# Kernel optimization log

Measured on AMD Instinct MI355X. Metric: run time of the kernel, lower is better.

Reference implementation:

```python
import jax, jax.numpy as jnp
import numpy as np

WS = 7           # window size (module init window_size=(7,7))
HEADS = 8
LN_EPS = 1e-5


def _relative_position_index(ws: int) -> np.ndarray:
    # Exactly mirrors the torch buffer construction in __init__.
    ch = np.arange(ws)
    coords = np.stack(np.meshgrid(ch, ch, indexing='ij'))          # [2, ws, ws]
    cf = coords.reshape(2, -1)                                     # [2, ws*ws]
    rel = cf[:, :, None] - cf[:, None, :]                          # [2, N, N]
    rel = rel.transpose(1, 2, 0).copy()                            # [N, N, 2]
    rel[:, :, 0] += ws - 1
    rel[:, :, 1] += ws - 1
    rel[:, :, 0] *= 2 * ws - 1
    return rel.sum(-1)                                             # [N, N] in [0, 169)


def setup_inputs() -> dict:
    key = jax.random.key(0)
    ks = jax.random.split(key, 5)
    B, H, W, C = 4, 224, 224, 256
    return {
        'x': jax.random.normal(ks[0], (B, H, W, C), jnp.float32),
        'w_qkv': jax.random.normal(ks[1], (C, 3 * C), jnp.float32) * 0.02,
        'b_qkv': jnp.zeros((3 * C,), jnp.float32),
        'bias_table': jax.random.normal(ks[2], ((2 * WS - 1) ** 2, HEADS), jnp.float32) * 0.02,
        'w_out': jax.random.normal(ks[3], (C, C), jnp.float32) * 0.02,
        'b_out': jnp.zeros((C,), jnp.float32),
        'ln_gamma': jnp.ones((C,), jnp.float32),
        'ln_beta': jnp.zeros((C,), jnp.float32),
    }


def reference(x, w_qkv, b_qkv, bias_table, w_out, b_out, ln_gamma, ln_beta):
    B, H, W, C = x.shape
    hd = C // HEADS
    scale = (HEADS // 2) ** -0.5          # faithful: head_dim = heads // 2 in source
    N = WS * WS

    # window partition: (B,H,W,C) -> (nW, WS*WS, C)
    xw = x.reshape(B, H // WS, WS, W // WS, WS, C)
    xw = xw.transpose(0, 1, 3, 2, 4, 5).reshape(-1, N, C)
    nW = xw.shape[0]

    # fused QKV projection
    qkv = xw @ w_qkv + b_qkv                                        # [nW, N, 3C]
    qkv = qkv.reshape(nW, N, 3, HEADS, hd).transpose(2, 0, 3, 1, 4)  # [3, nW, h, N, hd]
    q, k, v = qkv[0], qkv[1], qkv[2]

    # relative position bias gather: [N, N, heads] -> [heads, N, N]
    rel_idx = _relative_position_index(WS)                          # numpy constant
    bias = bias_table[rel_idx.reshape(-1)].reshape(N, N, HEADS).transpose(2, 0, 1)

    attn = jnp.einsum('whqd,whkd->whqk', q, k) * scale + bias[None]  # [nW, h, N, N]
    attn = jax.nn.softmax(attn, axis=-1)

    out = jnp.einsum('whqk,whkd->whqd', attn, v)                    # [nW, h, N, hd]
    out = out.transpose(0, 2, 1, 3).reshape(nW, N, C)
    out = out @ w_out + b_out

    # residual + layernorm (temporal_tokens + cur_tokens -> LayerNorm)
    y = out + xw
    mean = y.mean(-1, keepdims=True)
    var = ((y - mean) ** 2).mean(-1, keepdims=True)
    y = (y - mean) * jax.lax.rsqrt(var + LN_EPS) * ln_gamma + ln_beta
    return y.reshape(-1, C)                                          # [nW*N, C] tokens
```

## Files before the change

kernel.cpp:

```cpp
#include <hip/hip_runtime.h>
#include <hip/hip_bf16.h>

#define BATCH 4
#define IMG 224
#define CDIM 256
#define WS 7
#define NWIN 4096
#define NTOK 49
#define TTOK 200704
#define HEADS 8
#define HD 32
#define SCALE 0.5f
#define LN_EPS 1e-5f

typedef __attribute__((ext_vector_type(8))) short short8v;
typedef __attribute__((ext_vector_type(4))) float f32x4;
typedef unsigned short u16;

__device__ __forceinline__ u16 f2bf(float f) {
  __hip_bfloat16 h = __float2bfloat16(f);
  return *reinterpret_cast<u16*>(&h);
}

__device__ __forceinline__ void gld_lds16(const void* g, void* l) {
  __builtin_amdgcn_global_load_lds(
      (const __attribute__((address_space(1))) unsigned int*)g,
      (__attribute__((address_space(3))) unsigned int*)l, 16, 0, 0);
}

__global__ __launch_bounds__(256) void pack_x(const float* __restrict__ x,
                                              u16* __restrict__ xb) {
  const int NCH = TTOK * 32;
  for (int id = blockIdx.x * 256 + threadIdx.x; id < NCH; id += 2048 * 256) {
    int t = id >> 5;
    int cc = (id & 31) << 3;
    int wq = t / 49, n = t - wq * 49;
    int b = wq >> 10, rem = wq & 1023;
    int gh = (rem >> 5) * 7 + n / 7;
    int gw = (rem & 31) * 7 + n % 7;
    const float* src = x + (((size_t)b * IMG + gh) * IMG + gw) * CDIM + cc;
    float4 f0 = *(const float4*)src;
    float4 f1 = *(const float4*)(src + 4);
    union { u16 us[8]; uint4 v; } pk;
    pk.us[0] = f2bf(f0.x); pk.us[1] = f2bf(f0.y);
    pk.us[2] = f2bf(f0.z); pk.us[3] = f2bf(f0.w);
    pk.us[4] = f2bf(f1.x); pk.us[5] = f2bf(f1.y);
    pk.us[6] = f2bf(f1.z); pk.us[7] = f2bf(f1.w);
    *(uint4*)(xb + (size_t)id * 8) = pk.v;
  }
}

__global__ __launch_bounds__(256) void pack_w(const float* __restrict__ wqkv,
                                              const float* __restrict__ wout,
                                              u16* __restrict__ wqkvT,
                                              u16* __restrict__ woutT) {
  int id = blockIdx.x * 256 + threadIdx.x;
  if (id < 196608) {
    int nn = id >> 8, k = id & 255;
    wqkvT[id] = f2bf(wqkv[(size_t)k * 768 + nn]);
  } else {
    int id2 = id - 196608;
    int nn = id2 >> 8, k = id2 & 255;
    woutT[id2] = f2bf(wout[(size_t)k * 256 + nn]);
  }
}

__global__ __launch_bounds__(256) void qkv_gemm(const u16* __restrict__ xb,
                                                const u16* __restrict__ wqkvT,
                                                const float* __restrict__ bqkv,
                                                u16* __restrict__ qkvb) {
  __shared__ __align__(16) short As[2][4096];
  __shared__ __align__(16) short Bs[2][4096];

  int tid = threadIdx.x;
  int lane = tid & 63, wid = tid >> 6;
  int wm = wid >> 1, wn = wid & 1;
  int hb = blockIdx.x;
  int bid = (hb & 7) * 1176 + (hb >> 3);
  int mt = bid / 6, nt = bid % 6;
  int m0 = mt * 128, n0 = nt * 128;

  f32x4 zero = {0.f, 0.f, 0.f, 0.f};
  f32x4 acc[4][4];
#pragma unroll
  for (int m = 0; m < 4; ++m)
#pragma unroll
    for (int n = 0; n < 4; ++n) acc[m][n] = zero;

#define STAGE_K1(buf, k0)                                                \
  {                                                                      \
    _Pragma("unroll") for (int i = 0; i < 2; ++i) {                      \
      int c = i * 256 + tid;                                             \
      int l6 = c & 63;                                                   \
      int rr = ((c >> 6) << 4) + (l6 & 15);                              \
      int kk = (k0) + ((l6 >> 4) << 3);                                  \
      gld_lds16(xb + (size_t)(m0 + rr) * 256 + kk, &As[buf][c * 8]);     \
      gld_lds16(wqkvT + (size_t)(n0 + rr) * 256 + kk, &Bs[buf][c * 8]);  \
    }                                                                    \
  }

  STAGE_K1(0, 0);
  __syncthreads();

  int buf = 0;
  for (int ks = 0; ks < 8; ++ks) {
    if (ks < 7) STAGE_K1(buf ^ 1, (ks + 1) * 32);
    short8v af[4], bfv[4];
#pragma unroll
    for (int m = 0; m < 4; ++m)
      af[m] = *(const short8v*)&As[buf][((wm * 4 + m) * 64 + lane) * 8];
#pragma unroll
    for (int n = 0; n < 4; ++n)
      bfv[n] = *(const short8v*)&Bs[buf][((wn * 4 + n) * 64 + lane) * 8];
#pragma unroll
    for (int m = 0; m < 4; ++m)
#pragma unroll
      for (int n = 0; n < 4; ++n)
        acc[m][n] = __builtin_amdgcn_mfma_f32_16x16x32_bf16(af[m], bfv[n],
                                                            acc[m][n], 0, 0, 0);
    __syncthreads();
    buf ^= 1;
  }

  int fr = lane & 15, fq = lane >> 4;
#pragma unroll
  for (int n = 0; n < 4; ++n) {
    int c = n0 + wn * 64 + n * 16 + fr;
    float bias = bqkv[c];
    u16* plane = qkvb + (size_t)((c >> 8) * 8 + ((c >> 5) & 7)) * TTOK * 32;
    int d = c & 31;
#pragma unroll
    for (int m = 0; m < 4; ++m) {
      int t0 = m0 + wm * 64 + m * 16 + fq * 4;
#pragma unroll
      for (int r = 0; r < 4; ++r)
        plane[(size_t)(t0 + r) * 32 + d] = f2bf(acc[m][n][r] + bias);
    }
  }
}

__global__ __launch_bounds__(256) void attn_kernel(
    const u16* __restrict__ qkvb, const float* __restrict__ bias_table,
    u16* __restrict__ attnb) {
  __shared__ u16 Pl[4][4096];
  __shared__ u16 Vl[4][32 * 72];
  __shared__ float bsh[4][169];

  int bid = blockIdx.x;
  int w = bid >> 1;
  int wid = threadIdx.x >> 6, lane = threadIdx.x & 63;
  int h = ((bid & 1) << 2) | wid;
  int cl = lane & 15, cg = lane >> 4;

  for (int i = lane; i < 169; i += 64)
    bsh[wid][i] = bias_table[i * HEADS + h];

  const size_t wbase = (size_t)w * 49 * 32;
  const u16* qp = qkvb + (size_t)h * TTOK * 32 + wbase;
  const u16* kp = qkvb + (size_t)(8 + h) * TTOK * 32 + wbase;
  const u16* vp = qkvb + (size_t)(16 + h) * TTOK * 32 + wbase;

  short8v qf[4], kf[4];
#pragma unroll
  for (int mt = 0; mt < 4; ++mt) {
    int off = (mt * 16 + cl) * 32 + cg * 8;
    qf[mt] = *(const short8v*)(qp + off);
    kf[mt] = *(const short8v*)(kp + off);
  }

  short8v vz = {0, 0, 0, 0, 0, 0, 0, 0};
#pragma unroll
  for (int pass = 0; pass < 4; ++pass) {
    int cidx = pass * 64 + lane;
    int t = cidx >> 2, dc = (cidx & 3) * 8;
    short8v vv = (t < 49) ? *(const short8v*)(vp + t * 32 + dc) : vz;
#pragma unroll
    for (int j = 0; j < 8; ++j) Vl[wid][(dc + j) * 72 + t] = vv[j];
  }

  f32x4 zero4 = {0.f, 0.f, 0.f, 0.f};
  f32x4 s[4][4];
#pragma unroll
  for (int mt = 0; mt < 4; ++mt)
#pragma unroll
    for (int nt = 0; nt < 4; ++nt)
      s[mt][nt] = __builtin_amdgcn_mfma_f32_16x16x32_bf16(qf[mt], kf[nt],
                                                          zero4, 0, 0, 0);

  int kr7[4], kc7[4];
#pragma unroll
  for (int nt = 0; nt < 4; ++nt) {
    int col = nt * 16 + cl;
    kr7[nt] = (col * 9363) >> 16;
    kc7[nt] = col - kr7[nt] * 7;
  }

  f32x4 rinv[4];
#pragma unroll
  for (int mt = 0; mt < 4; ++mt) {
#pragma unroll
    for (int r = 0; r < 4; ++r) {
      int row = mt * 16 + cg * 4 + r;
      int qr = (row * 9363) >> 16;
      int qc = row - qr * 7;
      float sv[4];
#pragma unroll
      for (int nt = 0; nt < 4; ++nt) {
        int col = nt * 16 + cl;
        if (col < 49) {
          int idx = (qr - kr7[nt] + 6) * 13 + (qc - kc7[nt] + 6);
          sv[nt] = s[mt][nt][r] * SCALE + bsh[wid][idx];
        } else {
          sv[nt] = -1e30f;
        }
      }
      float m = fmaxf(fmaxf(sv[0], sv[1]), fmaxf(sv[2], sv[3]));
#pragma unroll
      for (int msk = 1; msk < 16; msk <<= 1) m = fmaxf(m, __shfl_xor(m, msk));
      float sum = 0.f;
#pragma unroll
      for (int nt = 0; nt < 4; ++nt) {
        float p = __expf(sv[nt] - m);
        s[mt][nt][r] = p;
        sum += p;
      }
#pragma unroll
      for (int msk = 1; msk < 16; msk <<= 1) sum += __shfl_xor(sum, msk);
      rinv[mt][r] = 1.0f / sum;
    }
  }

#pragma unroll
  for (int mt = 0; mt < 4; ++mt)
#pragma unroll
    for (int r = 0; r < 4; ++r) {
      int row = mt * 16 + cg * 4 + r;
      int swz = (row & 7) << 3;
#pragma unroll
      for (int nt = 0; nt < 4; ++nt) {
        int col = nt * 16 + cl;
        Pl[wid][(row * 64 + col) ^ swz] = f2bf(s[mt][nt][r]);
      }
    }

  f32x4 o[4][2];
#pragma unroll
  for (int mt = 0; mt < 4; ++mt)
#pragma unroll
    for (int nt2 = 0; nt2 < 2; ++nt2) o[mt][nt2] = zero4;

#pragma unroll
  for (int kt = 0; kt < 2; ++kt) {
    short8v vfr[2];
#pragma unroll
    for (int nt2 = 0; nt2 < 2; ++nt2)
      vfr[nt2] = *(const short8v*)&Vl[wid][(nt2 * 16 + cl) * 72 + kt * 32 + cg * 8];
#pragma unroll
    for (int mt = 0; mt < 4; ++mt) {
      int row = mt * 16 + cl;
      short8v pa = *(const short8v*)
          &Pl[wid][(row * 64 + kt * 32 + cg * 8) ^ ((row & 7) << 3)];
#pragma unroll
      for (int nt2 = 0; nt2 < 2; ++nt2)
        o[mt][nt2] = __builtin_amdgcn_mfma_f32_16x16x32_bf16(pa, vfr[nt2],
                                                             o[mt][nt2], 0, 0, 0);
    }
  }

#pragma unroll
  for (int mt = 0; mt < 4; ++mt)
#pragma unroll
    for (int r = 0; r < 4; ++r) {
      int row = mt * 16 + cg * 4 + r;
      if (row < 49) {
        float ri = rinv[mt][r];
        size_t dst = (size_t)(w * 49 + row) * 256 + h * 32;
#pragma unroll
        for (int nt2 = 0; nt2 < 2; ++nt2)
          attnb[dst + nt2 * 16 + cl] = f2bf(o[mt][nt2][r] * ri);
      }
    }
}

__global__ __launch_bounds__(512) void out_ln_kernel(
    const u16* __restrict__ attnb, const u16* __restrict__ woutT,
    const float* __restrict__ bout, const float* __restrict__ x,
    const float* __restrict__ gamma, const float* __restrict__ beta,
    float* __restrict__ out) {
  __shared__ __align__(16) short As[2][4096];
  __shared__ __align__(16) short Bs[2][8192];
  __shared__ float ls1[128], ls2[128];
  __shared__ int rowoff_s[128];

  int tid = threadIdx.x;
  int lane = tid & 63, wid = tid >> 6;
  int wm = wid >> 2, wn = wid & 3;
  int m0 = blockIdx.x * 128;

  if (tid < 128) {
    ls1[tid] = 0.f;
    ls2[tid] = 0.f;
    int t = m0 + tid;
    int wq = t / 49, n = t - wq * 49;
    int b = wq >> 10, rem = wq & 1023;
    int gh = (rem >> 5) * 7 + n / 7;
    int gw = (rem & 31) * 7 + n % 7;
    rowoff_s[tid] = ((b * IMG + gh) * IMG + gw) * CDIM;
  }

  f32x4 zero = {0.f, 0.f, 0.f, 0.f};
  f32x4 acc[4][4];
#pragma unroll
  for (int m = 0; m < 4; ++m)
#pragma unroll
    for (int n = 0; n < 4; ++n) acc[m][n] = zero;

#define STAGE_K3(buf, k0)                                                 \
  {                                                                       \
    {                                                                     \
      int c = tid;                                                        \
      int l6 = c & 63;                                                    \
      int rr = ((c >> 6) << 4) + (l6 & 15);                               \
      int kk = (k0) + ((l6 >> 4) << 3);                                   \
      gld_lds16(attnb + (size_t)(m0 + rr) * 256 + kk, &As[buf][c * 8]);   \
    }                                                                     \
    _Pragma("unroll") for (int i = 0; i < 2; ++i) {                       \
      int c = i * 512 + tid;                                              \
      int l6 = c & 63;                                                    \
      int cc = ((c >> 6) << 4) + (l6 & 15);                               \
      int kk = (k0) + ((l6 >> 4) << 3);                                   \
      gld_lds16(woutT + (size_t)cc * 256 + kk, &Bs[buf][c * 8]);          \
    }                                                                     \
  }

  STAGE_K3(0, 0);
  __syncthreads();

  int buf = 0;
  for (int ks = 0; ks < 8; ++ks) {
    if (ks < 7) STAGE_K3(buf ^ 1, (ks + 1) * 32);
    short8v af[4], bfv[4];
#pragma unroll
    for (int m = 0; m < 4; ++m)
      af[m] = *(const short8v*)&As[buf][((wm * 4 + m) * 64 + lane) * 8];
#pragma unroll
    for (int n = 0; n < 4; ++n)
      bfv[n] = *(const short8v*)&Bs[buf][((wn * 4 + n) * 64 + lane) * 8];
#pragma unroll
    for (int m = 0; m < 4; ++m)
#pragma unroll
      for (int n = 0; n < 4; ++n)
        acc[m][n] = __builtin_amdgcn_mfma_f32_16x16x32_bf16(af[m], bfv[n],
                                                            acc[m][n], 0, 0, 0);
    __syncthreads();
    buf ^= 1;
  }

  int fr = lane & 15, fq = lane >> 4;
#pragma unroll
  for (int m = 0; m < 4; ++m) {
#pragma unroll
    for (int r = 0; r < 4; ++r) {
      int lrow = wm * 64 + m * 16 + fq * 4 + r;
      const float* xr = x + rowoff_s[lrow];
      float s1 = 0.f, s2 = 0.f;
#pragma unroll
      for (int n = 0; n < 4; ++n) {
        int c = wn * 64 + n * 16 + fr;
        float v = acc[m][n][r] + bout[c] + xr[c];
        acc[m][n][r] = v;
        s1 += v;
        s2 += v * v;
      }
#pragma unroll
      for (int off = 1; off < 16; off <<= 1) {
        s1 += __shfl_xor(s1, off);
        s2 += __shfl_xor(s2, off);
      }
      if (fr == 0) {
        atomicAdd(&ls1[lrow], s1);
        atomicAdd(&ls2[lrow], s2);
      }
    }
  }
  __syncthreads();

#pragma unroll
  for (int m = 0; m < 4; ++m) {
#pragma unroll
    for (int r = 0; r < 4; ++r) {
      int lrow = wm * 64 + m * 16 + fq * 4 + r;
      float mean = ls1[lrow] * (1.0f / 256.0f);
      float var = ls2[lrow] * (1.0f / 256.0f) - mean * mean;
      float rstd = rsqrtf(var + LN_EPS);
      size_t orow = (size_t)(m0 + lrow) * 256;
#pragma unroll
      for (int n = 0; n < 4; ++n) {
        int c = wn * 64 + n * 16 + fr;
        out[orow + c] = (acc[m][n][r] - mean) * rstd * gamma[c] + beta[c];
      }
    }
  }
}

extern "C" void kernel_launch(void* const* d_in, const int* in_sizes, int n_in,
                              void* d_out, int out_size, void* d_ws, size_t ws_size,
                              hipStream_t stream) {
  const float* x     = (const float*)d_in[0];
  const float* wqkv  = (const float*)d_in[1];
  const float* bqkv  = (const float*)d_in[2];
  const float* btab  = (const float*)d_in[3];
  const float* wout  = (const float*)d_in[4];
  const float* bout  = (const float*)d_in[5];
  const float* gamma = (const float*)d_in[6];
  const float* beta  = (const float*)d_in[7];
  float* out = (float*)d_out;

  u16* qkvb  = (u16*)d_ws;
  u16* xb    = qkvb + (size_t)24 * TTOK * 32;
  u16* attnb = xb;
  u16* wqkvT = xb + (size_t)TTOK * 256;
  u16* woutT = wqkvT + 196608;

  pack_x<<<2048, 256, 0, stream>>>(x, xb);
  pack_w<<<1024, 256, 0, stream>>>(wqkv, wout, wqkvT, woutT);
  qkv_gemm<<<(TTOK / 128) * 6, 256, 0, stream>>>(xb, wqkvT, bqkv, qkvb);
  attn_kernel<<<NWIN * 2, 256, 0, stream>>>(qkvb, btab, attnb);
  out_ln_kernel<<<TTOK / 128, 512, 0, stream>>>(attnb, woutT, bout, x, gamma,
                                                beta, out);
}
```

Before: 922.6 us.

## Store QKV row-major with packed vector stores and preload full K in LDS

The QKV GEMM now swaps operand roles so each lane holds four consecutive output columns, which allows packed 8-byte stores into a token-major [token,768] QKV buffer instead of scattered 2-byte stores into per-head planes. The attention kernel is updated to read Q/K/V with a 768-element row stride. The GEMM also loads the whole K=256 extent into 128KB of LDS up front and drops the double-buffered pipeline and per-step barriers. This costs occupancy and removes load/compute overlap, and the attention loads become strided across rows.

Result: slower. 978.6 us (+6.1%).

```diff
diff --git a/kernel.cpp b/kernel.cpp
--- a/kernel.cpp
+++ b/kernel.cpp
@@ -69,72 +69,70 @@
                                                 const u16* __restrict__ wqkvT,
                                                 const float* __restrict__ bqkv,
                                                 u16* __restrict__ qkvb) {
-  __shared__ __align__(16) short As[2][4096];
-  __shared__ __align__(16) short Bs[2][4096];
+  __shared__ __align__(16) short As[32768];
+  __shared__ __align__(16) short Bs[32768];
 
   int tid = threadIdx.x;
   int lane = tid & 63, wid = tid >> 6;
-  int wm = wid >> 1, wn = wid & 1;
+  int wn = wid >> 1, wt = wid & 1;
   int hb = blockIdx.x;
   int bid = (hb & 7) * 1176 + (hb >> 3);
   int mt = bid / 6, nt = bid % 6;
   int m0 = mt * 128, n0 = nt * 128;
 
+#pragma unroll
+  for (int ks = 0; ks < 8; ++ks) {
+#pragma unroll
+    for (int i = 0; i < 2; ++i) {
+      int c = i * 256 + tid;
+      int l6 = c & 63;
+      int rr = ((c >> 6) << 4) + (l6 & 15);
+      int kk = ks * 32 + ((l6 >> 4) << 3);
+      gld_lds16(wqkvT + (size_t)(n0 + rr) * 256 + kk, &As[ks * 4096 + c * 8]);
+      gld_lds16(xb + (size_t)(m0 + rr) * 256 + kk, &Bs[ks * 4096 + c * 8]);
+    }
+  }
+
   f32x4 zero = {0.f, 0.f, 0.f, 0.f};
   f32x4 acc[4][4];
 #pragma unroll
-  for (int m = 0; m < 4; ++m)
-#pragma unroll
-    for (int n = 0; n < 4; ++n) acc[m][n] = zero;
-
-#define STAGE_K1(buf, k0)                                                \
-  {                                                                      \
-    _Pragma("unroll") for (int i = 0; i < 2; ++i) {                      \
-      int c = i * 256 + tid;                                             \
-      int l6 = c & 63;                                                   \
-      int rr = ((c >> 6) << 4) + (l6 & 15);                              \
-      int kk = (k0) + ((l6 >> 4) << 3);                                  \
-      gld_lds16(xb + (size_t)(m0 + rr) * 256 + kk, &As[buf][c * 8]);     \
-      gld_lds16(wqkvT + (size_t)(n0 + rr) * 256 + kk, &Bs[buf][c * 8]);  \
-    }                                                                    \
-  }
-
-  STAGE_K1(0, 0);
+  for (int n = 0; n < 4; ++n)
+#pragma unroll
+    for (int t = 0; t < 4; ++t) acc[n][t] = zero;
+
   __syncthreads();
 
-  int buf = 0;
+#pragma unroll
   for (int ks = 0; ks < 8; ++ks) {
-    if (ks < 7) STAGE_K1(buf ^ 1, (ks + 1) * 32);
     short8v af[4], bfv[4];
 #pragma unroll
-    for (int m = 0; m < 4; ++m)
-      af[m] = *(const short8v*)&As[buf][((wm * 4 + m) * 64 + lane) * 8];
-#pragma unroll
     for (int n = 0; n < 4; ++n)
-      bfv[n] = *(const short8v*)&Bs[buf][((wn * 4 + n) * 64 + lane) * 8];
-#pragma unroll
-    for (int m = 0; m < 4; ++m)
-#pragma unroll
-      for (int n = 0; n < 4; ++n)
-        acc[m][n] = __builtin_amdgcn_mfma_f32_16x16x32_bf16(af[m], bfv[n],
-                                                            acc[m][n], 0, 0, 0);
-    __syncthreads();
-    buf ^= 1;
-  }
-
-  int fr = lane & 15, fq = lane >> 4;
+      af[n] = *(const short8v*)&As[ks * 4096 + ((wn * 4 + n) * 64 + lane) * 8];
+#pragma unroll
+    for (int t = 0; t < 4; ++t)
+      bfv[t] = *(const short8v*)&Bs[ks * 4096 + ((wt * 4 + t) * 64 + lane) * 8];
+#pragma unroll
+    for (int n = 0; n < 4; ++n)
+#pragma unroll
+      for (int t = 0; t < 4; ++t)
+        acc[n][t] = __builtin_amdgcn_mfma_f32_16x16x32_bf16(af[n], bfv[t],
+                                                            acc[n][t], 0, 0, 0);
+  }
+
+  int cl = lane & 15, fq = lane >> 4;
 #pragma unroll
   for (int n = 0; n < 4; ++n) {
-    int c = n0 + wn * 64 + n * 16 + fr;
-    float bias = bqkv[c];
-    u16* plane = qkvb + (size_t)((c >> 8) * 8 + ((c >> 5) & 7)) * TTOK * 32;
-    int d = c & 31;
-#pragma unroll
-    for (int m = 0; m < 4; ++m) {
-      int t0 = m0 + wm * 64 + m * 16 + fq * 4;
-#pragma unroll
-      for (int r = 0; r < 4; ++r)
-        plane[(size_t)(t0 + r) * 32 + d] = f2bf(acc[m][n][r] + bias);
+    int nb = n0 + wn * 64 + n * 16 + fq * 4;
+    float4 bq = *(const float4*)(bqkv + nb);
+#pragma unroll
+    for (int t = 0; t < 4; ++t) {
+      int tr = m0 + wt * 64 + t * 16 + cl;
+      union { u16 us[4]; uint2 v; } pk;
+      pk.us[0] = f2bf(acc[n][t][0] + bq.x);
+      pk.us[1] = f2bf(acc[n][t][1] + bq.y);
+      pk.us[2] = f2bf(acc[n][t][2] + bq.z);
+      pk.us[3] = f2bf(acc[n][t][3] + bq.w);
+      *(uint2*)(qkvb + (size_t)tr * 768 + nb) = pk.v;
     }
   }
 }
@@ -155,15 +153,15 @@
   for (int i = lane; i < 169; i += 64)
     bsh[wid][i] = bias_table[i * HEADS + h];
 
-  const size_t wbase = (size_t)w * 49 * 32;
-  const u16* qp = qkvb + (size_t)h * TTOK * 32 + wbase;
-  const u16* kp = qkvb + (size_t)(8 + h) * TTOK * 32 + wbase;
-  const u16* vp = qkvb + (size_t)(16 + h) * TTOK * 32 + wbase;
+  const u16* rowb = qkvb + (size_t)w * 49 * 768;
+  const u16* qp = rowb + h * 32;
+  const u16* kp = rowb + 256 + h * 32;
+  const u16* vp = rowb + 512 + h * 32;
 
   short8v qf[4], kf[4];
 #pragma unroll
   for (int mt = 0; mt < 4; ++mt) {
-    int off = (mt * 16 + cl) * 32 + cg * 8;
+    int off = (mt * 16 + cl) * 768 + cg * 8;
     qf[mt] = *(const short8v*)(qp + off);
     kf[mt] = *(const short8v*)(kp + off);
   }
@@ -173,7 +171,7 @@
   for (int pass = 0; pass < 4; ++pass) {
     int cidx = pass * 64 + lane;
     int t = cidx >> 2, dc = (cidx & 3) * 8;
-    short8v vv = (t < 49) ? *(const short8v*)(vp + t * 32 + dc) : vz;
+    short8v vv = (t < 49) ? *(const short8v*)(vp + (size_t)t * 768 + dc) : vz;
 #pragma unroll
     for (int j = 0; j < 8; ++j) Vl[wid][(dc + j) * 72 + t] = vv[j];
   }
@@ -417,7 +415,7 @@
   float* out = (float*)d_out;
 
   u16* qkvb  = (u16*)d_ws;
-  u16* xb    = qkvb + (size_t)24 * TTOK * 32;
+  u16* xb    = qkvb + (size_t)TTOK * 768;
   u16* attnb = xb;
   u16* wqkvT = xb + (size_t)TTOK * 256;
   u16* woutT = wqkvT + 196608;
```
